# Optimization experiments

Hardware: AMD Instinct MI355X
Metric: run time of the kernel (lower is better)

The kernel has to match this reference:

```python
import jax, jax.numpy as jnp
import numpy as np
from jax import lax

N_NODES = 32768   # 256 graphs x 128 nodes
N_GRAPHS = 256
DEG = 16          # fixed neighbor-list length per node
IN = 128
HID = 256
OUT = 16


def setup_inputs() -> dict:
    key = jax.random.key(0)
    ks = jax.random.split(key, 12)
    g = lambda k, s: jax.random.normal(k, s, dtype=jnp.float32) * 0.05
    return {
        "x": jax.random.normal(ks[0], (N_NODES, IN), dtype=jnp.float32),
        "neighbors": jax.random.randint(ks[1], (N_NODES, DEG), 0, N_NODES, dtype=jnp.int32),
        # conv1: LSTM(in=128, hid=128), fc_self/fc_neigh 128->256
        "Wi1": g(ks[2], (4 * IN, IN)),
        "Wh1": g(ks[3], (4 * IN, IN)),
        "bi1": jnp.zeros((4 * IN,), jnp.float32),
        "bh1": jnp.zeros((4 * IN,), jnp.float32),
        "Ws1": g(ks[4], (HID, IN)),
        "Wn1": g(ks[5], (HID, IN)),
        "b1": jnp.zeros((HID,), jnp.float32),
        # conv2: LSTM(in=256, hid=256), fc_self/fc_neigh 256->256
        "Wi2": g(ks[6], (4 * HID, HID)),
        "Wh2": g(ks[7], (4 * HID, HID)),
        "bi2": jnp.zeros((4 * HID,), jnp.float32),
        "bh2": jnp.zeros((4 * HID,), jnp.float32),
        "Ws2": g(ks[8], (HID, HID)),
        "Wn2": g(ks[9], (HID, HID)),
        "b2": jnp.zeros((HID,), jnp.float32),
        # classifier 256 -> 16
        "Wc": g(ks[10], (OUT, HID)),
        "bc": jnp.zeros((OUT,), jnp.float32),
    }


def _lstm_agg(h, neighbors, Wi, Wh, bi, bh):
    # DGL SAGEConv 'lstm' reducer: LSTM over each node's neighbor feature
    # sequence, hidden size == feature size; returns final hidden state.
    # h: [N, F], neighbors: [N, D]
    N, F = h.shape

    def step(carry, nbr_t):
        hs, cs = carry
        x = h[nbr_t]                                  # [N, F] gather
        gates = x @ Wi.T + hs @ Wh.T + (bi + bh)      # [N, 4F]
        i, f, g, o = jnp.split(gates, 4, axis=-1)     # PyTorch gate order
        c = jax.nn.sigmoid(f) * cs + jax.nn.sigmoid(i) * jnp.tanh(g)
        hn = jax.nn.sigmoid(o) * jnp.tanh(c)
        return (hn, c), None

    z = jnp.zeros((N, F), h.dtype)
    (hT, _), _ = lax.scan(step, (z, z), neighbors.T)  # scan over DEG steps
    return hT


def _sage_conv(h, neighbors, Wi, Wh, bi, bh, Ws, Wn, b):
    h_neigh = _lstm_agg(h, neighbors, Wi, Wh, bi, bh)
    return h @ Ws.T + h_neigh @ Wn.T + b


def reference(x, neighbors, Wi1, Wh1, bi1, bh1, Ws1, Wn1, b1,
              Wi2, Wh2, bi2, bh2, Ws2, Wn2, b2, Wc, bc):
    h = _sage_conv(x, neighbors, Wi1, Wh1, bi1, bh1, Ws1, Wn1, b1)
    h = jax.nn.relu(h)
    h = _sage_conv(h, neighbors, Wi2, Wh2, bi2, bh2, Ws2, Wn2, b2)
    h = jax.nn.relu(h)
    # dgl.mean_nodes over a batch of equal-size graphs
    hg = h.reshape(N_GRAPHS, N_NODES // N_GRAPHS, HID).mean(axis=1)  # [B, HID]
    return hg @ Wc.T + bc                                            # [B, OUT]
```

## Files before the change

### kernel.cpp

```cpp
#include <hip/hip_runtime.h>

#define N_NODES 32768
#define DEG 16
#define IN_F 128
#define HIDF 256
#define N_GRAPHS 256
#define NPG 128
#define OUT_F 16

typedef unsigned short u16;
typedef unsigned int u32;
typedef __bf16 bf16x8 __attribute__((ext_vector_type(8)));
typedef float f32x4 __attribute__((ext_vector_type(4)));
typedef u16 u16x4 __attribute__((ext_vector_type(4)));
typedef u16 u16x8 __attribute__((ext_vector_type(8)));

__device__ __forceinline__ u16 f2bf(float f) {
  union { float f; unsigned u; } v; v.f = f;
  return (u16)((v.u + 0x7FFFu + ((v.u >> 16) & 1u)) >> 16);
}
__device__ __forceinline__ float bf2f(u16 b) {
  union { unsigned u; float f; } v; v.u = ((unsigned)b) << 16;
  return v.f;
}
__device__ __forceinline__ float sigm(float x) { return 1.0f / (1.0f + __expf(-x)); }
__device__ __forceinline__ float tanhfast(float x) {
  float e = __expf(2.0f * x);
  return (e - 1.0f) / (e + 1.0f);
}


__global__ void k_prep_x(const float* __restrict__ x, u16* __restrict__ out, int n4) {
  int i = blockIdx.x * blockDim.x + threadIdx.x;
  if (i < n4) {
    float4 v = ((const float4*)x)[i];
    ushort4 o;
    o.x = f2bf(v.x); o.y = f2bf(v.y); o.z = f2bf(v.z); o.w = f2bf(v.w);
    ((ushort4*)out)[i] = o;
  }
}

__global__ void k_prep_wg(const float* __restrict__ Wi, const float* __restrict__ Wh,
                          const float* __restrict__ bi, const float* __restrict__ bh,
                          u16* __restrict__ Wip, u16* __restrict__ Whp,
                          float* __restrict__ bwp, int F) {
  int total = 4 * F * F;
  for (int idx = blockIdx.x * blockDim.x + threadIdx.x; idx < total;
       idx += gridDim.x * blockDim.x) {
    int p = idx / F, k = idx % F;
    {
      int fe = p >> 2, g = p & 3;
      int orig = g * F + fe;
      Whp[idx] = f2bf(Wh[orig * F + k]);
    }
    {
      int base = p & ~63, local = p & 63;
      int lq = local >> 4, mt = (local >> 2) & 3, gate = local & 3;
      int oldp = base + mt * 16 + lq * 4 + gate;
      int fe = oldp >> 2, g = oldp & 3;
      int orig = g * F + fe;
      Wip[idx] = f2bf(Wi[orig * F + k]);
      if (k == 0) bwp[p] = bi[orig] + bh[orig];
    }
  }
}

__global__ void k_prep_cast(const float* __restrict__ Ws, const float* __restrict__ Wn,
                            u16* __restrict__ Bs, u16* __restrict__ Bn, int n) {
  int i = blockIdx.x * blockDim.x + threadIdx.x;
  if (i < n) { Bs[i] = f2bf(Ws[i]); Bn[i] = f2bf(Wn[i]); }
}

template <int K, int NC>
__launch_bounds__(256, 4)
__global__ void k_gemm(const u16* __restrict__ A, const u16* __restrict__ B,
                       const float* __restrict__ bias, u16* __restrict__ C) {
  constexpr int ROWB = 2 * K;
  __shared__ u16 lds[64 * K];
  char* ldsb = (char*)lds;
  const int tid = threadIdx.x;
  const int w = tid >> 6;
  const int lane = tid & 63;
  const int l16 = lane & 15, lq = lane >> 4;
  const int row0 = blockIdx.x * 64;
  const int col0 = blockIdx.y * 128;

  constexpr int CH = K / 8;
  constexpr int RPI = 256 / CH;
#pragma unroll
  for (int it = 0; it < 64 / RPI; ++it) {
    int r = tid / CH + it * RPI;
    int ch = tid % CH;
    bf16x8 v = *(const bf16x8*)(A + (size_t)(row0 + r) * K + ch * 8);
    int bo = r * ROWB + ((ch * 16) ^ ((r & 7) << 4));
    *(bf16x8*)(ldsb + bo) = v;
  }
  __syncthreads();

  f32x4 acc[4][2];
#pragma unroll
  for (int mt = 0; mt < 4; ++mt)
#pragma unroll
    for (int nt = 0; nt < 2; ++nt)
#pragma unroll
      for (int j = 0; j < 4; ++j) acc[mt][nt][j] = 0.f;

  for (int ks = 0; ks < K / 32; ++ks) {
    bf16x8 a[4];
#pragma unroll
    for (int mt = 0; mt < 4; ++mt) {
      int r = mt * 16 + l16;
      int bo = r * ROWB + (((ks * 32 + lq * 8) * 2) ^ ((r & 7) << 4));
      a[mt] = *(const bf16x8*)(ldsb + bo);
    }
#pragma unroll
    for (int nt = 0; nt < 2; ++nt) {
      int coln = col0 + w * 32 + nt * 16 + l16;
      bf16x8 b = *(const bf16x8*)(B + (size_t)coln * K + ks * 32 + lq * 8);
#pragma unroll
      for (int mt = 0; mt < 4; ++mt)
        acc[mt][nt] = __builtin_amdgcn_mfma_f32_16x16x32_bf16(a[mt], b, acc[mt][nt], 0, 0, 0);
    }
  }
#pragma unroll
  for (int mt = 0; mt < 4; ++mt)
#pragma unroll
    for (int nt = 0; nt < 2; ++nt) {
      int coln = col0 + w * 32 + nt * 16 + l16;
      float bb = bias[coln];
#pragma unroll
      for (int j = 0; j < 4; ++j) {
        int r = row0 + mt * 16 + lq * 4 + j;
        C[(size_t)r * NC + coln] = f2bf(acc[mt][nt][j] + bb);
      }
    }
}

template <int K>
__launch_bounds__(256, 4)
__global__ void k_comb(const u16* __restrict__ A, const u16* __restrict__ B,
                       const u16* __restrict__ XS, u16* __restrict__ C) {
  constexpr int ROWB = 2 * K;
  __shared__ u16 lds[64 * K];
  char* ldsb = (char*)lds;
  const int tid = threadIdx.x;
  const int w = tid >> 6;
  const int lane = tid & 63;
  const int l16 = lane & 15, lq = lane >> 4;
  const int row0 = blockIdx.x * 64;
  const int col0 = blockIdx.y * 128;

  constexpr int CH = K / 8;
  constexpr int RPI = 256 / CH;
#pragma unroll
  for (int it = 0; it < 64 / RPI; ++it) {
    int r = tid / CH + it * RPI;
    int ch = tid % CH;
    bf16x8 v = *(const bf16x8*)(A + (size_t)(row0 + r) * K + ch * 8);
    int bo = r * ROWB + ((ch * 16) ^ ((r & 7) << 4));
    *(bf16x8*)(ldsb + bo) = v;
  }
  __syncthreads();

  f32x4 acc[4][2];
#pragma unroll
  for (int mt = 0; mt < 4; ++mt)
#pragma unroll
    for (int nt = 0; nt < 2; ++nt)
#pragma unroll
      for (int j = 0; j < 4; ++j) acc[mt][nt][j] = 0.f;

  for (int ks = 0; ks < K / 32; ++ks) {
    bf16x8 a[4];
#pragma unroll
    for (int mt = 0; mt < 4; ++mt) {
      int r = mt * 16 + l16;
      int bo = r * ROWB + (((ks * 32 + lq * 8) * 2) ^ ((r & 7) << 4));
      a[mt] = *(const bf16x8*)(ldsb + bo);
    }
#pragma unroll
    for (int nt = 0; nt < 2; ++nt) {
      int coln = col0 + w * 32 + nt * 16 + l16;
      bf16x8 b = *(const bf16x8*)(B + (size_t)coln * K + ks * 32 + lq * 8);
#pragma unroll
      for (int mt = 0; mt < 4; ++mt)
        acc[mt][nt] = __builtin_amdgcn_mfma_f32_16x16x32_bf16(a[mt], b, acc[mt][nt], 0, 0, 0);
    }
  }
#pragma unroll
  for (int mt = 0; mt < 4; ++mt)
#pragma unroll
    for (int nt = 0; nt < 2; ++nt) {
      int coln = col0 + w * 32 + nt * 16 + l16;
#pragma unroll
      for (int j = 0; j < 4; ++j) {
        int r = row0 + mt * 16 + lq * 4 + j;
        float v = acc[mt][nt][j] + bf2f(XS[(size_t)r * HIDF + coln]);
        C[(size_t)r * HIDF + coln] = f2bf(fmaxf(v, 0.f));
      }
    }
}

template <int F>
__launch_bounds__(512, 2)
__global__ void k_layer(const u16* __restrict__ XW,
                        const u16* __restrict__ Whp,
                        const int* __restrict__ nbr,
                        u16* __restrict__ hout) {
  constexpr int NT = 64;
  constexpr int KS = F / 32;
  constexpr int ROWB = 2 * F;
  __shared__ __align__(16) u16 Wst[8 * 64 * F];
  __shared__ __align__(16) u16 hbuf[NT * F];
  __shared__ int snbrT[DEG * NT];
  const int tid = threadIdx.x;
  const int w = tid >> 6;
  const int lane = tid & 63;
  const int l16 = lane & 15, lq = lane >> 4;
  const int nodeg = blockIdx.x * NT;
  const int row0 = w * 64;

#pragma unroll
  for (int it = 0; it < 16; ++it) {
    int idx = it * 512 + tid;
    int r = idx >> 4;
    int ch = idx & 15;
    bf16x8 v = *(const bf16x8*)(Whp + (size_t)r * F + ch * 8);
    int s = r >> 6, rr = r & 63;
    char* base = (char*)Wst + (size_t)s * (64 * ROWB);
    int bo = rr * ROWB + ((ch * 16) ^ ((rr & 7) << 4));
    *(bf16x8*)(base + bo) = v;
  }
  for (int idx = tid; idx < DEG * NT; idx += 512) {
    int nl = idx / DEG, tt = idx % DEG;
    snbrT[tt * NT + nl] = nbr[(size_t)(nodeg + nl) * DEG + tt];
  }

  float c[4][4];
#pragma unroll
  for (int mt = 0; mt < 4; ++mt)
#pragma unroll
    for (int nt = 0; nt < 4; ++nt) c[mt][nt] = 0.f;

  __syncthreads();

  const char* wb = (const char*)Wst + (size_t)w * (64 * ROWB);
  const char* hb = (const char*)hbuf;
  char* hw = (char*)hbuf;

#pragma unroll 1
  for (int t = 0; t < DEG; ++t) {
    u16x8 xwv[4][2];
#pragma unroll
    for (int nt = 0; nt < 4; ++nt) {
      int nb = snbrT[t * NT + nt * 16 + l16];
      const u16* bp = XW + (size_t)nb * (4 * F) + row0 + lq * 16;
      xwv[nt][0] = *(const u16x8*)(bp);
      xwv[nt][1] = *(const u16x8*)(bp + 8);
    }

    f32x4 acc[4][4];
#pragma unroll
    for (int mt = 0; mt < 4; ++mt)
#pragma unroll
      for (int nt = 0; nt < 4; ++nt)
#pragma unroll
        for (int j = 0; j < 4; ++j) acc[mt][nt][j] = 0.f;

    __syncthreads();
    if (t > 0) {
#pragma unroll
      for (int ks = 0; ks < KS; ++ks) {
        bf16x8 a[4];
#pragma unroll
        for (int mt = 0; mt < 4; ++mt) {
          int rr = mt * 16 + l16;
          int bo = rr * ROWB + (((ks * 32 + lq * 8) * 2) ^ ((rr & 7) << 4));
          a[mt] = *(const bf16x8*)(wb + bo);
        }
        bf16x8 b[4];
#pragma unroll
        for (int nt = 0; nt < 4; ++nt) {
          int nl = nt * 16 + l16;
          int bo = nl * ROWB + (((ks * 32 + lq * 8) * 2) ^ ((nl & 7) << 4));
          b[nt] = *(const bf16x8*)(hb + bo);
        }
#pragma unroll
        for (int mt = 0; mt < 4; ++mt)
#pragma unroll
          for (int nt = 0; nt < 4; ++nt)
            acc[mt][nt] = __builtin_amdgcn_mfma_f32_16x16x32_bf16(a[mt], b[nt], acc[mt][nt], 0, 0, 0);
      }
    }
    __syncthreads();

#pragma unroll
    for (int mt = 0; mt < 4; ++mt) {
      int fe = w * 16 + mt * 4 + lq;
      const int h2 = mt >> 1, q4 = (mt & 1) * 4;
#pragma unroll
      for (int nt = 0; nt < 4; ++nt) {
        int nl = nt * 16 + l16;
        float pi = acc[mt][nt][0] + bf2f(xwv[nt][h2][q4 + 0]);
        float pf = acc[mt][nt][1] + bf2f(xwv[nt][h2][q4 + 1]);
        float pg = acc[mt][nt][2] + bf2f(xwv[nt][h2][q4 + 2]);
        float po = acc[mt][nt][3] + bf2f(xwv[nt][h2][q4 + 3]);
        float cn = sigm(pf) * c[mt][nt] + sigm(pi) * tanhfast(pg);
        c[mt][nt] = cn;
        float hn = sigm(po) * tanhfast(cn);
        int bo = nl * ROWB + ((fe * 2) ^ ((nl & 7) << 4));
        *(u16*)(hw + bo) = f2bf(hn);
      }
    }
  }
  __syncthreads();

  constexpr int CPN = F / 8;
  for (int idx = tid; idx < NT * CPN; idx += 512) {
    int nl = idx / CPN, fg = idx % CPN;
    int bo = nl * ROWB + ((fg * 16) ^ ((nl & 7) << 4));
    u16x8 v = *(const u16x8*)(hb + bo);
    *(u16x8*)(hout + (size_t)(nodeg + nl) * F + fg * 8) = v;
  }
}

template <int F, bool T0>
__launch_bounds__(512, 4)
__global__ void k_step(const u16* __restrict__ hprev,
                       const u16* __restrict__ XW,
                       const u16* __restrict__ Whp,
                       const int* __restrict__ nbr,
                       int t,
                       u16* __restrict__ cT,
                       u16* __restrict__ hnext) {
  constexpr int ROWB = 2 * F;
  constexpr int KS = F / 32;
  constexpr int RBN = F / 16;
  __shared__ __align__(16) u16 Alds[64 * F];
  __shared__ __align__(16) u16 tl[256 * 24];
  char* ldsb = (char*)Alds;
  const int tid = threadIdx.x;
  const int w = tid >> 6;
  const int lane = tid & 63;
  const int l16 = lane & 15, lq = lane >> 4;

  const int p = blockIdx.x + RBN * blockIdx.y;
  const int s = p >> 3;
  const int rb = s % RBN;
  const int g = (p & 7) + 8 * (s / RBN);

  const int row0 = rb * 64;
  const int col0 = g * 256;
  const int feb = row0 >> 2;
  const int n0 = col0 + w * 32 + l16;
  const int n1 = n0 + 16;

  const int nb0 = nbr[(size_t)n0 * DEG + t];
  const int nb1 = nbr[(size_t)n1 * DEG + t];

  if constexpr (!T0) {
    constexpr int CH = F / 8;
    constexpr int RPI = 512 / CH;
#pragma unroll
    for (int it = 0; it < 64 / RPI; ++it) {
      int r = tid / CH + it * RPI;
      int ch = tid % CH;
      bf16x8 v = *(const bf16x8*)(Whp + (size_t)(row0 + r) * F + ch * 8);
      int bo = r * ROWB + ((ch * 16) ^ ((r & 7) << 4));
      *(bf16x8*)(ldsb + bo) = v;
    }
  }

  u16x8 xwv[2][2];
  {
    const u16* b0 = XW + (size_t)nb0 * (4 * F) + row0 + lq * 16;
    const u16* b1 = XW + (size_t)nb1 * (4 * F) + row0 + lq * 16;
    xwv[0][0] = *(const u16x8*)(b0);
    xwv[0][1] = *(const u16x8*)(b0 + 8);
    xwv[1][0] = *(const u16x8*)(b1);
    xwv[1][1] = *(const u16x8*)(b1 + 8);
  }

  float cold[4][2];
  if constexpr (!T0) {
#pragma unroll
    for (int mt = 0; mt < 4; ++mt) {
      cold[mt][0] = bf2f(cT[(size_t)(feb + mt * 4 + lq) * N_NODES + n0]);
      cold[mt][1] = bf2f(cT[(size_t)(feb + mt * 4 + lq) * N_NODES + n1]);
    }
  }

  f32x4 acc[4][2];
#pragma unroll
  for (int mt = 0; mt < 4; ++mt)
#pragma unroll
    for (int nt = 0; nt < 2; ++nt)
#pragma unroll
      for (int j = 0; j < 4; ++j) acc[mt][nt][j] = 0.f;

  if constexpr (!T0) {
    __syncthreads();
    const u16* hb0 = hprev + (size_t)n0 * F + lq * 8;
    const u16* hb1 = hprev + (size_t)n1 * F + lq * 8;
#pragma unroll
    for (int ks = 0; ks < KS; ++ks) {
      bf16x8 b0 = *(const bf16x8*)(hb0 + ks * 32);
      bf16x8 b1 = *(const bf16x8*)(hb1 + ks * 32);
      bf16x8 a[4];
#pragma unroll
      for (int mt = 0; mt < 4; ++mt) {
        int r = mt * 16 + l16;
        int bo = r * ROWB + (((ks * 32 + lq * 8) * 2) ^ ((r & 7) << 4));
        a[mt] = *(const bf16x8*)(ldsb + bo);
      }
#pragma unroll
      for (int mt = 0; mt < 4; ++mt) {
        acc[mt][0] = __builtin_amdgcn_mfma_f32_16x16x32_bf16(a[mt], b0, acc[mt][0], 0, 0, 0);
        acc[mt][1] = __builtin_amdgcn_mfma_f32_16x16x32_bf16(a[mt], b1, acc[mt][1], 0, 0, 0);
      }
    }
  }

#pragma unroll
  for (int mt = 0; mt < 4; ++mt) {
    int fe = feb + mt * 4 + lq;
#pragma unroll
    for (int nt = 0; nt < 2; ++nt) {
      int n = nt ? n1 : n0;
      float pi, pf, pg, po;
      if (mt < 2) {
        pi = acc[mt][nt][0] + bf2f(xwv[nt][0][(mt & 1) * 4 + 0]);
        pf = acc[mt][nt][1] + bf2f(xwv[nt][0][(mt & 1) * 4 + 1]);
        pg = acc[mt][nt][2] + bf2f(xwv[nt][0][(mt & 1) * 4 + 2]);
        po = acc[mt][nt][3] + bf2f(xwv[nt][0][(mt & 1) * 4 + 3]);
      } else {
        pi = acc[mt][nt][0] + bf2f(xwv[nt][1][(mt & 1) * 4 + 0]);
        pf = acc[mt][nt][1] + bf2f(xwv[nt][1][(mt & 1) * 4 + 1]);
        pg = acc[mt][nt][2] + bf2f(xwv[nt][1][(mt & 1) * 4 + 2]);
        po = acc[mt][nt][3] + bf2f(xwv[nt][1][(mt & 1) * 4 + 3]);
      }
      float cn;
      if constexpr (T0) cn = sigm(pi) * tanhfast(pg);
      else              cn = sigm(pf) * cold[mt][nt] + sigm(pi) * tanhfast(pg);
      float hn = sigm(po) * tanhfast(cn);
      cT[(size_t)fe * N_NODES + n] = f2bf(cn);
      tl[(w * 32 + nt * 16 + l16) * 24 + mt * 4 + lq] = f2bf(hn);
    }
  }
  __syncthreads();
  {
    int nloc = tid >> 1, q = tid & 1;
    u16x8 v = *(const u16x8*)&tl[nloc * 24 + q * 8];
    *(u16x8*)(hnext + (size_t)(col0 + nloc) * F + feb + q * 8) = v;
  }
}

__global__ void k_pool(const u16* __restrict__ h2, const float* __restrict__ Wc,
                       const float* __restrict__ bc, float* __restrict__ out) {
  __shared__ float hg[HIDF];
  int g = blockIdx.x;
  int tid = threadIdx.x;
  float s = 0.0f;
  for (int i = 0; i < NPG; ++i) s += bf2f(h2[(size_t)(g * NPG + i) * HIDF + tid]);
  hg[tid] = s * (1.0f / NPG);
  __syncthreads();
  if (tid < OUT_F) {
    float o = bc[tid];
    for (int fe = 0; fe < HIDF; ++fe) o += hg[fe] * Wc[tid * HIDF + fe];
    out[g * OUT_F + tid] = o;
  }
}

extern "C" void kernel_launch(void* const* d_in, const int* in_sizes, int n_in,
                              void* d_out, int out_size, void* d_ws, size_t ws_size,
                              hipStream_t stream) {
  const float* x   = (const float*)d_in[0];
  const int*   nbr = (const int*)d_in[1];
  const float* Wi1 = (const float*)d_in[2];
  const float* Wh1 = (const float*)d_in[3];
  const float* bi1 = (const float*)d_in[4];
  const float* bh1 = (const float*)d_in[5];
  const float* Ws1 = (const float*)d_in[6];
  const float* Wn1 = (const float*)d_in[7];
  const float* b1  = (const float*)d_in[8];
  const float* Wi2 = (const float*)d_in[9];
  const float* Wh2 = (const float*)d_in[10];
  const float* bi2 = (const float*)d_in[11];
  const float* bh2 = (const float*)d_in[12];
  const float* Ws2 = (const float*)d_in[13];
  const float* Wn2 = (const float*)d_in[14];
  const float* b2  = (const float*)d_in[15];
  const float* Wc  = (const float*)d_in[16];
  const float* bc  = (const float*)d_in[17];
  float* out = (float*)d_out;

  char* ws = (char*)d_ws;
  const size_t MB = 1u << 20;
  u16*   x16 = (u16*)(ws + 0);
  u16*   XW1 = (u16*)(ws + 8 * MB);
  u16*   XS1 = (u16*)(ws + 40 * MB);
  u16*   X2  = XS1;
  u16*   hA1 = (u16*)(ws + 56 * MB);
  u16*   XW2 = (u16*)(ws + 80 * MB);
  u16*   XS2 = (u16*)(ws + 0);
  u16*   h2o = XS2;
  u16*   hA2 = (u16*)(ws + 16 * MB);
  u16*   hB2 = (u16*)(ws + 32 * MB);
  u16*   c2  = (u16*)(ws + 56 * MB);
  char* wr = ws + 144 * MB;
  size_t off = 0;
  auto alloc = [&](size_t bytes) { void* p = wr + off; off += (bytes + 255) & ~(size_t)255; return p; };
  u16*   Wip1 = (u16*)alloc(512 * 128 * 2);
  u16*   Whp1 = (u16*)alloc(512 * 128 * 2);
  float* bwp1 = (float*)alloc(512 * 4);
  u16*   Bs1  = (u16*)alloc(256 * 128 * 2);
  u16*   Bn1  = (u16*)alloc(256 * 128 * 2);
  u16*   Wip2 = (u16*)alloc(1024 * 256 * 2);
  u16*   Whp2 = (u16*)alloc(1024 * 256 * 2);
  float* bwp2 = (float*)alloc(1024 * 4);
  u16*   Bs2  = (u16*)alloc(256 * 256 * 2);
  u16*   Bn2  = (u16*)alloc(256 * 256 * 2);

  k_prep_x<<<dim3(N_NODES * IN_F / 4 / 256), dim3(256), 0, stream>>>(x, x16, N_NODES * IN_F / 4);
  k_prep_wg<<<dim3(256), dim3(256), 0, stream>>>(Wi1, Wh1, bi1, bh1, Wip1, Whp1, bwp1, IN_F);
  k_prep_wg<<<dim3(1024), dim3(256), 0, stream>>>(Wi2, Wh2, bi2, bh2, Wip2, Whp2, bwp2, HIDF);
  k_prep_cast<<<dim3(128), dim3(256), 0, stream>>>(Ws1, Wn1, Bs1, Bn1, 256 * 128);
  k_prep_cast<<<dim3(256), dim3(256), 0, stream>>>(Ws2, Wn2, Bs2, Bn2, 256 * 256);

  k_gemm<128, 512><<<dim3(N_NODES / 64, 4), dim3(256), 0, stream>>>(x16, Wip1, bwp1, XW1);
  k_gemm<128, 256><<<dim3(N_NODES / 64, 2), dim3(256), 0, stream>>>(x16, Bs1, b1, XS1);
  k_layer<IN_F><<<dim3(N_NODES / 64), dim3(512), 0, stream>>>(XW1, Whp1, nbr, hA1);
  k_comb<128><<<dim3(N_NODES / 64, 2), dim3(256), 0, stream>>>(hA1, Bn1, XS1, X2);

  k_gemm<256, 1024><<<dim3(N_NODES / 64, 8), dim3(256), 0, stream>>>(X2, Wip2, bwp2, XW2);
  k_gemm<256, 256><<<dim3(N_NODES / 64, 2), dim3(256), 0, stream>>>(X2, Bs2, b2, XS2);
  {
    k_step<HIDF, true><<<dim3(16, N_NODES / 256), dim3(512), 0, stream>>>(
        hA2, XW2, Whp2, nbr, 0, c2, hA2);
    u16* hc = hA2; u16* hn = hB2;
    for (int t = 1; t < DEG; ++t) {
      k_step<HIDF, false><<<dim3(16, N_NODES / 256), dim3(512), 0, stream>>>(
          hc, XW2, Whp2, nbr, t, c2, hn);
      u16* tmp = hc; hc = hn; hn = tmp;
    }
    k_comb<256><<<dim3(N_NODES / 64, 2), dim3(256), 0, stream>>>(hc, Bn2, XS2, h2o);
  }

  k_pool<<<dim3(N_GRAPHS), dim3(256), 0, stream>>>(h2o, Wc, bc, out);
}
```

Measured before the change: 1.161 ms.

## Fuse layer-1 input projection into LSTM kernel with prefetched neighbor gathers

Drops the separate layer-1 XW GEMM, so each LSTM step now gathers raw 128-wide neighbor features into shared memory and computes x@Wi with MFMA, using Wi fragments held in registers and the bias folded into the accumulator init. The next step's neighbor rows are prefetched into registers while the current step computes, and the Wi weight permutation is turned off for layer 1. This removes a large intermediate write/read (512-wide gathered rows) in exchange for extra MFMA work per step and higher register pressure.

```diff
diff --git a/kernel.cpp b/kernel.cpp
--- a/kernel.cpp
+++ b/kernel.cpp
@@ -43,7 +43,7 @@
 __global__ void k_prep_wg(const float* __restrict__ Wi, const float* __restrict__ Wh,
                           const float* __restrict__ bi, const float* __restrict__ bh,
                           u16* __restrict__ Wip, u16* __restrict__ Whp,
-                          float* __restrict__ bwp, int F) {
+                          float* __restrict__ bwp, int F, int perm) {
   int total = 4 * F * F;
   for (int idx = blockIdx.x * blockDim.x + threadIdx.x; idx < total;
        idx += gridDim.x * blockDim.x) {
@@ -54,9 +54,12 @@
       Whp[idx] = f2bf(Wh[orig * F + k]);
     }
     {
-      int base = p & ~63, local = p & 63;
-      int lq = local >> 4, mt = (local >> 2) & 3, gate = local & 3;
-      int oldp = base + mt * 16 + lq * 4 + gate;
+      int oldp = p;
+      if (perm) {
+        int base = p & ~63, local = p & 63;
+        int lq = local >> 4, mt = (local >> 2) & 3, gate = local & 3;
+        oldp = base + mt * 16 + lq * 4 + gate;
+      }
       int fe = oldp >> 2, g = oldp & 3;
       int orig = g * F + fe;
       Wip[idx] = f2bf(Wi[orig * F + k]);
@@ -203,8 +206,10 @@
 
 template <int F>
 __launch_bounds__(512, 2)
-__global__ void k_layer(const u16* __restrict__ XW,
+__global__ void k_layer(const u16* __restrict__ X,
+                        const u16* __restrict__ Wip,
                         const u16* __restrict__ Whp,
+                        const float* __restrict__ bwp,
                         const int* __restrict__ nbr,
                         u16* __restrict__ hout) {
   constexpr int NT = 64;
@@ -212,7 +217,7 @@
   constexpr int ROWB = 2 * F;
   __shared__ __align__(16) u16 Wst[8 * 64 * F];
   __shared__ __align__(16) u16 hbuf[NT * F];
-  __shared__ int snbrT[DEG * NT];
+  __shared__ __align__(16) u16 xst[NT * F];
   const int tid = threadIdx.x;
   const int w = tid >> 6;
   const int lane = tid & 63;
@@ -231,10 +236,18 @@
     int bo = rr * ROWB + ((ch * 16) ^ ((rr & 7) << 4));
     *(bf16x8*)(base + bo) = v;
   }
-  for (int idx = tid; idx < DEG * NT; idx += 512) {
-    int nl = idx / DEG, tt = idx % DEG;
-    snbrT[tt * NT + nl] = nbr[(size_t)(nodeg + nl) * DEG + tt];
-  }
+
+  bf16x8 awi[4][KS];
+#pragma unroll
+  for (int mt = 0; mt < 4; ++mt)
+#pragma unroll
+    for (int ks = 0; ks < KS; ++ks)
+      awi[mt][ks] = *(const bf16x8*)(Wip + (size_t)(row0 + mt * 16 + l16) * F + ks * 32 + lq * 8);
+
+  f32x4 bw[4];
+#pragma unroll
+  for (int mt = 0; mt < 4; ++mt)
+    bw[mt] = *(const f32x4*)(bwp + row0 + mt * 16 + lq * 4);
 
   float c[4][4];
 #pragma unroll
@@ -242,32 +255,58 @@
 #pragma unroll
     for (int nt = 0; nt < 4; ++nt) c[mt][nt] = 0.f;
 
+#pragma unroll
+  for (int rep = 0; rep < 2; ++rep) {
+    int cidx = rep * 512 + tid;
+    int nl = cidx >> 4, ch = cidx & 15;
+    int nb = nbr[(size_t)(nodeg + nl) * DEG + 0];
+    bf16x8 v = *(const bf16x8*)(X + (size_t)nb * F + ch * 8);
+    int bo = nl * ROWB + ((ch * 16) ^ ((nl & 7) << 4));
+    *(bf16x8*)((char*)xst + bo) = v;
+  }
   __syncthreads();
 
   const char* wb = (const char*)Wst + (size_t)w * (64 * ROWB);
   const char* hb = (const char*)hbuf;
   char* hw = (char*)hbuf;
+  const char* xb = (const char*)xst;
+  char* xw = (char*)xst;
 
 #pragma unroll 1
   for (int t = 0; t < DEG; ++t) {
-    u16x8 xwv[4][2];
-#pragma unroll
-    for (int nt = 0; nt < 4; ++nt) {
-      int nb = snbrT[t * NT + nt * 16 + l16];
-      const u16* bp = XW + (size_t)nb * (4 * F) + row0 + lq * 16;
-      xwv[nt][0] = *(const u16x8*)(bp);
-      xwv[nt][1] = *(const u16x8*)(bp + 8);
+    bf16x8 xp[2];
+    const bool pf = (t + 1 < DEG);
+    if (pf) {
+#pragma unroll
+      for (int rep = 0; rep < 2; ++rep) {
+        int cidx = rep * 512 + tid;
+        int nl = cidx >> 4, ch = cidx & 15;
+        int nb = nbr[(size_t)(nodeg + nl) * DEG + (t + 1)];
+        xp[rep] = *(const bf16x8*)(X + (size_t)nb * F + ch * 8);
+      }
     }
 
     f32x4 acc[4][4];
 #pragma unroll
     for (int mt = 0; mt < 4; ++mt)
 #pragma unroll
-      for (int nt = 0; nt < 4; ++nt)
-#pragma unroll
-        for (int j = 0; j < 4; ++j) acc[mt][nt][j] = 0.f;
-
-    __syncthreads();
+      for (int nt = 0; nt < 4; ++nt) acc[mt][nt] = bw[mt];
+
+#pragma unroll
+    for (int ks = 0; ks < KS; ++ks) {
+      bf16x8 b[4];
+#pragma unroll
+      for (int nt = 0; nt < 4; ++nt) {
+        int nl = nt * 16 + l16;
+        int bo = nl * ROWB + (((ks * 32 + lq * 8) * 2) ^ ((nl & 7) << 4));
+        b[nt] = *(const bf16x8*)(xb + bo);
+      }
+#pragma unroll
+      for (int mt = 0; mt < 4; ++mt)
+#pragma unroll
+        for (int nt = 0; nt < 4; ++nt)
+          acc[mt][nt] = __builtin_amdgcn_mfma_f32_16x16x32_bf16(awi[mt][ks], b[nt], acc[mt][nt], 0, 0, 0);
+    }
     if (t > 0) {
 #pragma unroll
       for (int ks = 0; ks < KS; ++ks) {
@@ -297,23 +336,31 @@
 #pragma unroll
     for (int mt = 0; mt < 4; ++mt) {
       int fe = w * 16 + mt * 4 + lq;
-      const int h2 = mt >> 1, q4 = (mt & 1) * 4;
 #pragma unroll
       for (int nt = 0; nt < 4; ++nt) {
         int nl = nt * 16 + l16;
-        float pi = acc[mt][nt][0] + bf2f(xwv[nt][h2][q4 + 0]);
-        float pf = acc[mt][nt][1] + bf2f(xwv[nt][h2][q4 + 1]);
-        float pg = acc[mt][nt][2] + bf2f(xwv[nt][h2][q4 + 2]);
-        float po = acc[mt][nt][3] + bf2f(xwv[nt][h2][q4 + 3]);
-        float cn = sigm(pf) * c[mt][nt] + sigm(pi) * tanhfast(pg);
+        float pi = acc[mt][nt][0];
+        float pf2 = acc[mt][nt][1];
+        float pg = acc[mt][nt][2];
+        float po = acc[mt][nt][3];
+        float cn = sigm(pf2) * c[mt][nt] + sigm(pi) * tanhfast(pg);
         c[mt][nt] = cn;
         float hn = sigm(po) * tanhfast(cn);
         int bo = nl * ROWB + ((fe * 2) ^ ((nl & 7) << 4));
         *(u16*)(hw + bo) = f2bf(hn);
       }
     }
-  }
-  __syncthreads();
+    if (pf) {
+#pragma unroll
+      for (int rep = 0; rep < 2; ++rep) {
+        int cidx = rep * 512 + tid;
+        int nl = cidx >> 4, ch = cidx & 15;
+        int bo = nl * ROWB + ((ch * 16) ^ ((nl & 7) << 4));
+        *(bf16x8*)(xw + bo) = xp[rep];
+      }
+    }
+    __syncthreads();
+  }
 
   constexpr int CPN = F / 8;
   for (int idx = tid; idx < NT * CPN; idx += 512) {
@@ -497,7 +544,6 @@
   char* ws = (char*)d_ws;
   const size_t MB = 1u << 20;
   u16*   x16 = (u16*)(ws + 0);
-  u16*   XW1 = (u16*)(ws + 8 * MB);
   u16*   XS1 = (u16*)(ws + 40 * MB);
   u16*   X2  = XS1;
   u16*   hA1 = (u16*)(ws + 56 * MB);
@@ -522,14 +568,13 @@
   u16*   Bn2  = (u16*)alloc(256 * 256 * 2);
 
   k_prep_x<<<dim3(N_NODES * IN_F / 4 / 256), dim3(256), 0, stream>>>(x, x16, N_NODES * IN_F / 4);
-  k_prep_wg<<<dim3(256), dim3(256), 0, stream>>>(Wi1, Wh1, bi1, bh1, Wip1, Whp1, bwp1, IN_F);
-  k_prep_wg<<<dim3(1024), dim3(256), 0, stream>>>(Wi2, Wh2, bi2, bh2, Wip2, Whp2, bwp2, HIDF);
+  k_prep_wg<<<dim3(256), dim3(256), 0, stream>>>(Wi1, Wh1, bi1, bh1, Wip1, Whp1, bwp1, IN_F, 0);
+  k_prep_wg<<<dim3(1024), dim3(256), 0, stream>>>(Wi2, Wh2, bi2, bh2, Wip2, Whp2, bwp2, HIDF, 1);
   k_prep_cast<<<dim3(128), dim3(256), 0, stream>>>(Ws1, Wn1, Bs1, Bn1, 256 * 128);
   k_prep_cast<<<dim3(256), dim3(256), 0, stream>>>(Ws2, Wn2, Bs2, Bn2, 256 * 256);
 
-  k_gemm<128, 512><<<dim3(N_NODES / 64, 4), dim3(256), 0, stream>>>(x16, Wip1, bwp1, XW1);
   k_gemm<128, 256><<<dim3(N_NODES / 64, 2), dim3(256), 0, stream>>>(x16, Bs1, b1, XS1);
-  k_layer<IN_F><<<dim3(N_NODES / 64), dim3(512), 0, stream>>>(XW1, Whp1, nbr, hA1);
+  k_layer<IN_F><<<dim3(N_NODES / 64), dim3(512), 0, stream>>>(x16, Wip1, Whp1, bwp1, nbr, hA1);
   k_comb<128><<<dim3(N_NODES / 64, 2), dim3(256), 0, stream>>>(hA1, Bn1, XS1, X2);
 
   k_gemm<256, 1024><<<dim3(N_NODES / 64, 8), dim3(256), 0, stream>>>(X2, Wip2, bwp2, XW2);
```

Result: no change. 1.156 ms (median of 2 runs) (-0.5%).
